# Performance work log

Hardware: AMD Instinct MI355X
Metric: run time of the kernel (lower is better)

Reference implementation:

```python
import jax, jax.numpy as jnp
import numpy as np

B, D, T, R = 8, 128, 32768, 2
C = D // R  # reduced channel dim = 64


def conv1x1(x, w, b):
    # x: [B, Cin, T], w: [Cout, Cin], b: [Cout] -> [B, Cout, T]
    return jnp.einsum('oi,bit->bot', w, x) + b[None, :, None]


def setup_inputs() -> dict:
    key = jax.random.key(0)
    ks = jax.random.split(key, 16)
    inp = {
        'x1': jax.random.normal(ks[0], (B, D, T), dtype=jnp.float32),
        'x2': jnp.zeros((B, D, T), dtype=jnp.float32),  # unused in encoder stage
        'mask': jnp.ones((B, 1, T), dtype=jnp.float32),
        # 1x1 conv projections (weights squeezed to [out, in])
        'wq': jax.random.normal(ks[1], (C, D), dtype=jnp.float32) * 0.05,
        'bq': jnp.zeros((C,), dtype=jnp.float32),
        'wk': jax.random.normal(ks[2], (C, D), dtype=jnp.float32) * 0.05,
        'bk': jnp.zeros((C,), dtype=jnp.float32),
        'wv': jax.random.normal(ks[3], (C, D), dtype=jnp.float32) * 0.05,
        'bv': jnp.zeros((C,), dtype=jnp.float32),
        # E, F: Linear(C -> C) with bias
        'we': jax.random.normal(ks[4], (C, C), dtype=jnp.float32) * 0.1,
        'be': jnp.zeros((C,), dtype=jnp.float32),
        'wf': jax.random.normal(ks[5], (C, C), dtype=jnp.float32) * 0.1,
        'bf': jnp.zeros((C,), dtype=jnp.float32),
        # output 1x1 conv: C -> D
        'wo': jax.random.normal(ks[6], (D, C), dtype=jnp.float32) * 0.05,
        'bo': jnp.zeros((D,), dtype=jnp.float32),
    }
    return inp


def reference(x1, x2, mask, wq, bq, wk, bk, wv, bv, we, be, wf, bf, wo, bo):
    # Q/K/V projections (encoder stage: value from x1; x2 unused)
    Q = conv1x1(x1, wq, bq)              # [B, C, T]
    K = conv1x1(x1, wk, bk)              # [B, C, T]
    V = conv1x1(x1, wv, bv)              # [B, C, T]
    # K = E(K^T): [B, T, C] @ we^T + be
    Kp = jnp.einsum('bct,oc->bto', K, we) + be  # [B, T, C]
    # S = Q @ Kp -> [B, C, C], scaled by sqrt(last dim)
    S = jnp.einsum('bct,btk->bck', Q, Kp)
    P = jax.nn.softmax(S / jnp.sqrt(jnp.asarray(S.shape[-1], S.dtype)), axis=-1)
    # dropout is identity in eval mode
    # V = (F(V^T))^T: [B, C, T]
    Vp = jnp.einsum('bct,oc->bot', V, wf) + bf[None, :, None]  # [B, C, T]
    out = jnp.einsum('bck,bkt->bct', P, Vp)  # [B, C, T]
    out = conv1x1(jax.nn.relu(out), wo, bo)  # [B, D, T]
    return out * mask[:, 0:1, :]
```

## Files before the change

kernel.cpp:

```cpp
#include <hip/hip_runtime.h>
#include <stdint.h>
#include <stddef.h>

#define B_ 8
#define D_ 128
#define T_ 32768
#define C_ 64
#define NCH_ 128

typedef __bf16 bf16;
typedef __bf16 bf16x4 __attribute__((ext_vector_type(4)));
typedef __bf16 bf16x8 __attribute__((ext_vector_type(8)));
typedef float f32x4 __attribute__((ext_vector_type(4)));
typedef float f32x16 __attribute__((ext_vector_type(16)));

__device__ __forceinline__ f32x16 zero16() {
  f32x16 z;
#pragma unroll
  for (int i = 0; i < 16; ++i) z[i] = 0.f;
  return z;
}

__global__ __launch_bounds__(256) void k0_zero(float* __restrict__ p, int n)
{
  int i = blockIdx.x * 256 + threadIdx.x;
  if (i < n) p[i] = 0.f;
}

__global__ __launch_bounds__(256, 4) void k1_gram(
    const float* __restrict__ x1,
    const float* __restrict__ we, const float* __restrict__ wk,
    const float* __restrict__ bk, const float* __restrict__ be,
    const float* __restrict__ wf, const float* __restrict__ wv,
    const float* __restrict__ bv, const float* __restrict__ bfv,
    const float* __restrict__ wo,
    float* __restrict__ G, float* __restrict__ r,
    float* __restrict__ wkp, float* __restrict__ wvp,
    float* __restrict__ bkp, float* __restrict__ bvp,
    bf16* __restrict__ wobf)
{
  const int blk = blockIdx.x;
  const int tid = threadIdx.x;
  const int ngram = B_ * NCH_;

  if (blk >= ngram) {
    const int wb = blk - ngram;
    if (wb < 64) {
      const float* wa  = (wb < 32) ? we : wf;
      const float* wb2 = (wb < 32) ? wk : wv;
      float* outw      = (wb < 32) ? wkp : wvp;
      const int idx = (wb & 31) * 256 + tid;
      const int o = idx >> 7, d = idx & 127;
      float s = 0.f;
      for (int c = 0; c < 64; ++c) s += wa[o * 64 + c] * wb2[c * 128 + d];
      outw[idx] = s;
      if (tid < 64) {
        if (wb == 0) {
          float t = 0.f;
          for (int c = 0; c < 64; ++c) t += we[tid * 64 + c] * bk[c];
          bkp[tid] = t + be[tid];
        } else if (wb == 32) {
          float t = 0.f;
          for (int c = 0; c < 64; ++c) t += wf[tid * 64 + c] * bv[c];
          bvp[tid] = t + bfv[tid];
        }
      }
    } else {
      const int idx = (wb - 64) * 256 + tid;
      wobf[idx] = (bf16)wo[idx];
    }
    return;
  }

  __shared__ bf16 x_s[128 * 72];

  const int b  = blk >> 7;
  const int ch = blk & (NCH_ - 1);
  const int t0 = ch * (T_ / NCH_);
  const int wave = tid >> 6, lane = tid & 63;
  const int lrow = lane & 31, lk = lane >> 5;
  const int qa = wave >> 1, qb = wave & 1;

  const float* xb = x1 + (size_t)b * D_ * T_;

  f32x16 acc00 = zero16(), acc01 = zero16(), acc10 = zero16(), acc11 = zero16();
  float rsum = 0.f;

  const int scol = (tid & 15) * 4;
  const int srow0 = tid >> 4;

  const bf16* A0  = &x_s[(64 * qa + lrow) * 72 + 8 * lk];
  const bf16* A1  = A0 + 32 * 72;
  const bf16* Bb0 = &x_s[(64 * qb + lrow) * 72 + 8 * lk];
  const bf16* Bb1 = Bb0 + 32 * 72;

  for (int s = 0; s < 4; ++s) {
    const int tb = t0 + s * 64;
    if (s) __syncthreads();
#pragma unroll
    for (int it = 0; it < 8; ++it) {
      const int row = it * 16 + srow0;
      f32x4 v = *(const f32x4*)(xb + (size_t)row * T_ + tb + scol);
      bf16x4 h;
#pragma unroll
      for (int j = 0; j < 4; ++j) h[j] = (bf16)v[j];
      *(bf16x4*)&x_s[row * 72 + scol] = h;
    }
    __syncthreads();
#pragma unroll
    for (int k = 0; k < 4; ++k) {
      bf16x8 fa0 = *(const bf16x8*)(A0 + 16 * k);
      bf16x8 fa1 = *(const bf16x8*)(A1 + 16 * k);
      bf16x8 fb0 = *(const bf16x8*)(Bb0 + 16 * k);
      bf16x8 fb1 = *(const bf16x8*)(Bb1 + 16 * k);
      bf16x8 own = qb ? fa1 : fa0;
#pragma unroll
      for (int j = 0; j < 8; ++j) rsum += (float)own[j];
      acc00 = __builtin_amdgcn_mfma_f32_32x32x16_bf16(fa0, fb0, acc00, 0, 0, 0);
      acc01 = __builtin_amdgcn_mfma_f32_32x32x16_bf16(fa0, fb1, acc01, 0, 0, 0);
      acc10 = __builtin_amdgcn_mfma_f32_32x32x16_bf16(fa1, fb0, acc10, 0, 0, 0);
      acc11 = __builtin_amdgcn_mfma_f32_32x32x16_bf16(fa1, fb1, acc11, 0, 0, 0);
    }
  }

  float* gb = G + (size_t)b * 16384;
#pragma unroll
  for (int rr = 0; rr < 16; ++rr) {
    const int rloc = (rr & 3) + 8 * (rr >> 2) + 4 * lk;
    const int r0 = 64 * qa + rloc, r1 = 64 * qa + 32 + rloc;
    const int c0 = 64 * qb + lrow, c1 = 64 * qb + 32 + lrow;
    atomicAdd(&gb[r0 * 128 + c0], acc00[rr]);
    atomicAdd(&gb[r0 * 128 + c1], acc01[rr]);
    atomicAdd(&gb[r1 * 128 + c0], acc10[rr]);
    atomicAdd(&gb[r1 * 128 + c1], acc11[rr]);
  }
  float rtot = rsum + __shfl_xor(rsum, 32, 64);
  if (lk == 0) atomicAdd(&r[b * 128 + 32 * wave + lrow], rtot);
}

__global__ __launch_bounds__(128) void k3_softmax(
    const float* __restrict__ wq, const float* __restrict__ bq,
    const float* __restrict__ G, const float* __restrict__ r,
    const float* __restrict__ wkp, const float* __restrict__ wvp,
    const float* __restrict__ bkp, const float* __restrict__ bvp,
    bf16* __restrict__ attw, float* __restrict__ attb)
{
  const int b = blockIdx.x >> 6, c = blockIdx.x & 63;
  const int tid = threadIdx.x;
  __shared__ float sM[128], sR[128], sQ[128], sP[64];
  __shared__ float sRed;

  const float* Gb = G + (size_t)b * 16384;
  const float* wqc = wq + c * 128;

  const float rv = r[b * 128 + tid];
  sR[tid] = rv;
  float m = 0.f;
  for (int j = 0; j < 128; ++j) m += wqc[j] * Gb[j * 128 + tid];
  sM[tid] = m;
  sQ[tid] = wqc[tid] * rv;
  __syncthreads();

  if (tid < 64) {
    float q2 = sQ[tid] + sQ[tid + 64];
#pragma unroll
    for (int off = 32; off; off >>= 1) q2 += __shfl_xor(q2, off, 64);
    if (tid == 0) sRed = q2;
  }
  __syncthreads();
  const float qr = sRed;
  const float bqc = bq[c];

  if (tid < 64) {
    const int k = tid;
    float s = 0.f, wkr = 0.f;
    for (int i = 0; i < 128; ++i) {
      const float w = wkp[k * 128 + i];
      s += sM[i] * w;
      wkr += sR[i] * w;
    }
    const float bk2 = bkp[k];
    float logit = (s + bqc * wkr + bk2 * qr + (float)T_ * bqc * bk2) * 0.125f;
    float mx = logit;
#pragma unroll
    for (int off = 32; off; off >>= 1) mx = fmaxf(mx, __shfl_xor(mx, off, 64));
    const float e = __expf(logit - mx);
    float sum = e;
#pragma unroll
    for (int off = 32; off; off >>= 1) sum += __shfl_xor(sum, off, 64);
    sP[k] = e / sum;
  }
  __syncthreads();

  {
    float aw = 0.f;
    for (int k = 0; k < 64; ++k) aw += sP[k] * wvp[k * 128 + tid];
    attw[((size_t)b * 64 + c) * 128 + tid] = (bf16)aw;
  }
  if (tid < 64) {
    float pb = sP[tid] * bvp[tid];
#pragma unroll
    for (int off = 32; off; off >>= 1) pb += __shfl_xor(pb, off, 64);
    if (tid == 0) attb[b * 64 + c] = pb;
  }
}

__global__ __launch_bounds__(256, 4) void k4_out(
    const float* __restrict__ x1, const float* __restrict__ mask,
    const bf16* __restrict__ wobf, const float* __restrict__ bo,
    const bf16* __restrict__ attw, const float* __restrict__ attb,
    float* __restrict__ out)
{
  __shared__ bf16 m1[128 * 72];
  __shared__ float bo_s[128];
  __shared__ float ab_s[64];

  const int b = blockIdx.x >> 8;
  const int t0 = (blockIdx.x & 255) << 7;
  const int tid = threadIdx.x;
  const int wave = tid >> 6, lane = tid & 63;
  const int lrow = lane & 31, lk = lane >> 5;
  const int tcol = 32 * wave + lrow;

  if (tid < 128) bo_s[tid] = bo[tid];
  if (tid < 64) ab_s[tid] = attb[b * 64 + tid];
  __syncthreads();

  const float* xc = x1 + (size_t)b * D_ * T_ + t0 + tcol;
  const bf16* awb = attw + (size_t)b * 8192;

  f32x16 p0 = zero16(), p1 = zero16();
#pragma unroll
  for (int k0 = 0; k0 < 8; ++k0) {
    bf16x8 a0 = *(const bf16x8*)(awb + (size_t)lrow * 128 + 16 * k0 + 8 * lk);
    bf16x8 a1 = *(const bf16x8*)(awb + (size_t)(32 + lrow) * 128 + 16 * k0 + 8 * lk);
    bf16x8 bx;
#pragma unroll
    for (int j = 0; j < 8; ++j)
      bx[j] = (bf16)xc[(size_t)(16 * k0 + 8 * lk + j) * T_];
    p0 = __builtin_amdgcn_mfma_f32_32x32x16_bf16(a0, bx, p0, 0, 0, 0);
    p1 = __builtin_amdgcn_mfma_f32_32x32x16_bf16(a1, bx, p1, 0, 0, 0);
  }
  bf16* mrow = &m1[tcol * 72];
#pragma unroll
  for (int rr = 0; rr < 16; ++rr) {
    const int row = (rr & 3) + 8 * (rr >> 2) + 4 * lk;
    mrow[row]      = (bf16)fmaxf(p0[rr] + ab_s[row], 0.f);
    mrow[32 + row] = (bf16)fmaxf(p1[rr] + ab_s[32 + row], 0.f);
  }

  f32x16 q0 = zero16(), q1 = zero16(), q2 = zero16(), q3 = zero16();
#pragma unroll
  for (int k0 = 0; k0 < 4; ++k0) {
    bf16x8 bm = *(const bf16x8*)(mrow + 16 * k0 + 8 * lk);
    bf16x8 w0 = *(const bf16x8*)(wobf + (size_t)(lrow) * 64 + 16 * k0 + 8 * lk);
    bf16x8 w1 = *(const bf16x8*)(wobf + (size_t)(32 + lrow) * 64 + 16 * k0 + 8 * lk);
    bf16x8 w2 = *(const bf16x8*)(wobf + (size_t)(64 + lrow) * 64 + 16 * k0 + 8 * lk);
    bf16x8 w3 = *(const bf16x8*)(wobf + (size_t)(96 + lrow) * 64 + 16 * k0 + 8 * lk);
    q0 = __builtin_amdgcn_mfma_f32_32x32x16_bf16(w0, bm, q0, 0, 0, 0);
    q1 = __builtin_amdgcn_mfma_f32_32x32x16_bf16(w1, bm, q1, 0, 0, 0);
    q2 = __builtin_amdgcn_mfma_f32_32x32x16_bf16(w2, bm, q2, 0, 0, 0);
    q3 = __builtin_amdgcn_mfma_f32_32x32x16_bf16(w3, bm, q3, 0, 0, 0);
  }

  const float mv = mask[(size_t)b * T_ + t0 + tcol];
  float* ob = out + (size_t)b * D_ * T_ + t0 + tcol;
#pragma unroll
  for (int rr = 0; rr < 16; ++rr) {
    const int row = (rr & 3) + 8 * (rr >> 2) + 4 * lk;
    ob[(size_t)(row) * T_]      = (q0[rr] + bo_s[row]) * mv;
    ob[(size_t)(32 + row) * T_] = (q1[rr] + bo_s[32 + row]) * mv;
    ob[(size_t)(64 + row) * T_] = (q2[rr] + bo_s[64 + row]) * mv;
    ob[(size_t)(96 + row) * T_] = (q3[rr] + bo_s[96 + row]) * mv;
  }
}

extern "C" void kernel_launch(void* const* d_in, const int* in_sizes, int n_in,
                              void* d_out, int out_size, void* d_ws, size_t ws_size,
                              hipStream_t stream)
{
  const float* x1   = (const float*)d_in[0];
  const float* mask = (const float*)d_in[2];
  const float* wq   = (const float*)d_in[3];
  const float* bq   = (const float*)d_in[4];
  const float* wk   = (const float*)d_in[5];
  const float* bk   = (const float*)d_in[6];
  const float* wv   = (const float*)d_in[7];
  const float* bv   = (const float*)d_in[8];
  const float* we   = (const float*)d_in[9];
  const float* be   = (const float*)d_in[10];
  const float* wf   = (const float*)d_in[11];
  const float* bfv  = (const float*)d_in[12];
  const float* wo   = (const float*)d_in[13];
  const float* bo   = (const float*)d_in[14];
  float* out = (float*)d_out;

  char* base = (char*)d_ws;
  size_t off = 0;
  float* G    = (float*)(base + off); off += (size_t)B_ * 16384 * 4;
  float* r    = (float*)(base + off); off += (size_t)B_ * 128 * 4;
  float* wkp  = (float*)(base + off); off += 8192 * 4;
  float* wvp  = (float*)(base + off); off += 8192 * 4;
  float* bkp  = (float*)(base + off); off += 64 * 4;
  float* bvp  = (float*)(base + off); off += 64 * 4;
  float* attb = (float*)(base + off); off += (size_t)B_ * 64 * 4;
  bf16* attw  = (bf16*)(base + off);  off += (size_t)B_ * 64 * 128 * 2;
  bf16* wobf  = (bf16*)(base + off);  off += 8192 * 2;

  const int nzero = B_ * 16384 + B_ * 128;
  k0_zero<<<(nzero + 255) / 256, 256, 0, stream>>>(G, nzero);
  k1_gram<<<B_ * NCH_ + 96, 256, 0, stream>>>(
      x1, we, wk, bk, be, wf, wv, bv, bfv, wo,
      G, r, wkp, wvp, bkp, bvp, wobf);
  k3_softmax<<<B_ * 64, 128, 0, stream>>>(wq, bq, G, r, wkp, wvp, bkp, bvp, attw, attb);
  k4_out<<<B_ * (T_ / 128), 256, 0, stream>>>(x1, mask, wobf, bo, attw, attb, out);
}
```

Before: 413.9 us.

## Replace Gram atomics with per-chunk partial buffers and a separate reduction kernel

Halves the number of time chunks per batch in the Gram kernel, so each block accumulates over twice as many timesteps. When the workspace is large enough, each block writes its partial 128x128 Gram tile to a dedicated buffer instead of issuing float atomicAdds into a shared per-batch matrix. A new reduction kernel then sums the partials into G. This is meant to remove atomic contention, at the cost of about 32 MB of extra partial-sum traffic, an extra launch, and fewer blocks for parallelism.

```diff
diff --git a/kernel.cpp b/kernel.cpp
--- a/kernel.cpp
+++ b/kernel.cpp
@@ -6,7 +6,7 @@
 #define D_ 128
 #define T_ 32768
 #define C_ 64
-#define NCH_ 128
+#define NCH_ 64
 
 typedef __bf16 bf16;
 typedef __bf16 bf16x4 __attribute__((ext_vector_type(4)));
@@ -37,7 +37,8 @@
     float* __restrict__ G, float* __restrict__ r,
     float* __restrict__ wkp, float* __restrict__ wvp,
     float* __restrict__ bkp, float* __restrict__ bvp,
-    bf16* __restrict__ wobf)
+    bf16* __restrict__ wobf,
+    float* __restrict__ gpart)
 {
   const int blk = blockIdx.x;
   const int tid = threadIdx.x;
@@ -74,7 +75,7 @@
 
   __shared__ bf16 x_s[128 * 72];
 
-  const int b  = blk >> 7;
+  const int b  = blk / NCH_;
   const int ch = blk & (NCH_ - 1);
   const int t0 = ch * (T_ / NCH_);
   const int wave = tid >> 6, lane = tid & 63;
@@ -94,7 +95,7 @@
   const bf16* Bb0 = &x_s[(64 * qb + lrow) * 72 + 8 * lk];
   const bf16* Bb1 = Bb0 + 32 * 72;
 
-  for (int s = 0; s < 4; ++s) {
+  for (int s = 0; s < 8; ++s) {
     const int tb = t0 + s * 64;
     if (s) __syncthreads();
 #pragma unroll
@@ -123,19 +124,46 @@
     }
   }
 
-  float* gb = G + (size_t)b * 16384;
-#pragma unroll
-  for (int rr = 0; rr < 16; ++rr) {
-    const int rloc = (rr & 3) + 8 * (rr >> 2) + 4 * lk;
-    const int r0 = 64 * qa + rloc, r1 = 64 * qa + 32 + rloc;
-    const int c0 = 64 * qb + lrow, c1 = 64 * qb + 32 + lrow;
-    atomicAdd(&gb[r0 * 128 + c0], acc00[rr]);
-    atomicAdd(&gb[r0 * 128 + c1], acc01[rr]);
-    atomicAdd(&gb[r1 * 128 + c0], acc10[rr]);
-    atomicAdd(&gb[r1 * 128 + c1], acc11[rr]);
+  if (gpart) {
+    float* gp = gpart + (size_t)blk * 16384;
+#pragma unroll
+    for (int rr = 0; rr < 16; ++rr) {
+      const int rloc = (rr & 3) + 8 * (rr >> 2) + 4 * lk;
+      const int r0 = 64 * qa + rloc, r1 = 64 * qa + 32 + rloc;
+      const int c0 = 64 * qb + lrow, c1 = 64 * qb + 32 + lrow;
+      gp[r0 * 128 + c0] = acc00[rr];
+      gp[r0 * 128 + c1] = acc01[rr];
+      gp[r1 * 128 + c0] = acc10[rr];
+      gp[r1 * 128 + c1] = acc11[rr];
+    }
+  } else {
+    float* gb = G + (size_t)b * 16384;
+#pragma unroll
+    for (int rr = 0; rr < 16; ++rr) {
+      const int rloc = (rr & 3) + 8 * (rr >> 2) + 4 * lk;
+      const int r0 = 64 * qa + rloc, r1 = 64 * qa + 32 + rloc;
+      const int c0 = 64 * qb + lrow, c1 = 64 * qb + 32 + lrow;
+      atomicAdd(&gb[r0 * 128 + c0], acc00[rr]);
+      atomicAdd(&gb[r0 * 128 + c1], acc01[rr]);
+      atomicAdd(&gb[r1 * 128 + c0], acc10[rr]);
+      atomicAdd(&gb[r1 * 128 + c1], acc11[rr]);
+    }
   }
   float rtot = rsum + __shfl_xor(rsum, 32, 64);
   if (lk == 0) atomicAdd(&r[b * 128 + 32 * wave + lrow], rtot);
+}
+
+__global__ __launch_bounds__(256) void k2_reduce(
+    const float* __restrict__ gpart, float* __restrict__ G)
+{
+  const int g4 = blockIdx.x * 256 + threadIdx.x;
+  const int b = g4 >> 12;
+  const int e4 = g4 & 4095;
+  const f32x4* p = (const f32x4*)(gpart + ((size_t)b * NCH_) * 16384) + e4;
+  f32x4 s = {0.f, 0.f, 0.f, 0.f};
+#pragma unroll
+  for (int ch = 0; ch < NCH_; ++ch) s += p[(size_t)ch * 4096];
+  *((f32x4*)G + g4) = s;
 }
 
 __global__ __launch_bounds__(128) void k3_softmax(
@@ -306,12 +334,19 @@
   float* attb = (float*)(base + off); off += (size_t)B_ * 64 * 4;
   bf16* attw  = (bf16*)(base + off);  off += (size_t)B_ * 64 * 128 * 2;
   bf16* wobf  = (bf16*)(base + off);  off += 8192 * 2;
+  off = (off + 15) & ~(size_t)15;
+  float* gpart = (float*)(base + off);
+  const size_t need = off + (size_t)B_ * NCH_ * 16384 * 4;
+  const bool use_part = (ws_size >= need);
+  if (!use_part) gpart = nullptr;
 
   const int nzero = B_ * 16384 + B_ * 128;
   k0_zero<<<(nzero + 255) / 256, 256, 0, stream>>>(G, nzero);
   k1_gram<<<B_ * NCH_ + 96, 256, 0, stream>>>(
       x1, we, wk, bk, be, wf, wv, bv, bfv, wo,
-      G, r, wkp, wvp, bkp, bvp, wobf);
+      G, r, wkp, wvp, bkp, bvp, wobf, gpart);
+  if (use_part)
+    k2_reduce<<<(B_ * 16384) / (256 * 4), 256, 0, stream>>>(gpart, G);
   k3_softmax<<<B_ * 64, 128, 0, stream>>>(wq, bq, G, r, wkp, wvp, bkp, bvp, attw, attb);
   k4_out<<<B_ * (T_ / 128), 256, 0, stream>>>(x1, mask, wobf, bo, attw, attb, out);
 }
```

Result: faster. 380.7 us (-8.0%).
